# Kernel tuning notes

Hardware: AMD Instinct MI355X
Metric: run time of the kernel (lower is better)

Reference implementation:

```python
import jax, jax.numpy as jnp
import numpy as np
from jax import lax

DN = ('NCHW', 'OIHW', 'NCHW')


def _conv(x, w, b, stride, pad):
    y = lax.conv_general_dilated(x, w, (stride, stride), [(pad, pad), (pad, pad)],
                                 dimension_numbers=DN)
    return y + b[None, :, None, None]


def _deconv(x, w, b, stride, pad):
    # torch ConvTranspose2d weight: (in, out, kH, kW). Equivalent forward conv:
    # flip spatially, swap in/out, dilate input by stride, pad by k-1-pad.
    k = w.shape[2]
    kern = jnp.flip(w, (2, 3)).transpose(1, 0, 2, 3)  # (out, in, kH, kW)
    p = k - 1 - pad
    y = lax.conv_general_dilated(x, kern, (1, 1), [(p, p), (p, p)],
                                 lhs_dilation=(stride, stride), dimension_numbers=DN)
    return y + b[None, :, None, None]


def setup_inputs() -> dict:
    key = jax.random.key(0)
    ks = jax.random.split(key, 16)
    s = 0.05
    D, K, H = 64, 512, 128  # embedding_dim, num_embeddings, hidden_channels
    inp = {
        'x': jax.random.uniform(ks[0], (16, 3, 256, 256), dtype=jnp.float32),
        'conv1_w': jax.random.normal(ks[1], (H, 3, 4, 4), jnp.float32) * s,
        'conv1_b': jnp.zeros((H,), jnp.float32),
        'conv2_w': jax.random.normal(ks[2], (H, H, 4, 4), jnp.float32) * s,
        'conv2_b': jnp.zeros((H,), jnp.float32),
        'conv3_w': jax.random.normal(ks[3], (D, H, 3, 3), jnp.float32) * s,
        'conv3_b': jnp.zeros((D,), jnp.float32),
        'emb': jax.random.normal(ks[4], (K, D), jnp.float32),
        'deconv1_w': jax.random.normal(ks[5], (D, H, 4, 4), jnp.float32) * s,
        'deconv1_b': jnp.zeros((H,), jnp.float32),
        'deconv2_w': jax.random.normal(ks[6], (H, H, 4, 4), jnp.float32) * s,
        'deconv2_b': jnp.zeros((H,), jnp.float32),
        'deconv3_w': jax.random.normal(ks[7], (H, 3, 3, 3), jnp.float32) * s,
        'deconv3_b': jnp.zeros((3,), jnp.float32),
    }
    return inp


def reference(x, conv1_w, conv1_b, conv2_w, conv2_b, conv3_w, conv3_b, emb,
              deconv1_w, deconv1_b, deconv2_w, deconv2_b, deconv3_w, deconv3_b):
    # Encoder
    h = jax.nn.relu(_conv(x, conv1_w, conv1_b, 2, 1))
    h = jax.nn.relu(_conv(h, conv2_w, conv2_b, 2, 1))
    z_e = _conv(h, conv3_w, conv3_b, 1, 1)  # (B, 64, 64, 64)

    # Vector quantizer (faithful to torch: flatten NCHW directly to (-1, D))
    D = emb.shape[1]
    flat = z_e.reshape(-1, D)  # (N, D)
    d = (jnp.sum(flat * flat, axis=1, keepdims=True)
         + jnp.sum(emb * emb, axis=1)
         - 2.0 * flat @ emb.T)  # (N, K)
    indices = jnp.argmin(d, axis=1)[:, None]  # (N, 1)
    z_q = emb[indices[:, 0]].reshape(z_e.shape)

    # Decoder
    g = jax.nn.relu(_deconv(z_q, deconv1_w, deconv1_b, 2, 1))
    g = jax.nn.relu(_deconv(g, deconv2_w, deconv2_b, 2, 1))
    x_recon = jax.nn.sigmoid(_deconv(g, deconv3_w, deconv3_b, 1, 1))
    return (x_recon, indices, z_q)
```

## Files before the change

### kernel.cpp

```cpp
#include <hip/hip_runtime.h>
#include <hip/hip_bf16.h>

#define DEV __device__ __forceinline__

typedef __attribute__((ext_vector_type(8))) short bf16x8;
typedef __attribute__((ext_vector_type(4))) float f32x4;
typedef __attribute__((ext_vector_type(4))) unsigned short u16x4;

#define MFMA16(a,b,c) __builtin_amdgcn_mfma_f32_16x16x32_bf16(a,b,c,0,0,0)

DEV unsigned short bfbits(float v){ __hip_bfloat16 h = __float2bfloat16(v); return *(unsigned short*)&h; }
DEV float bf2f(unsigned short u){ __hip_bfloat16 h = *(__hip_bfloat16*)&u; return __bfloat162float(h); }
DEV void split3(float v, unsigned short& h, unsigned short& m, unsigned short& l) {
  h = bfbits(v);        float r  = v - bf2f(h);
  m = bfbits(r);        float r2 = r - bf2f(m);
  l = bfbits(r2);
}
DEV uint4 zero4(){ uint4 z; z.x=0; z.y=0; z.z=0; z.w=0; return z; }
DEV void gload_lds16(const void* g, void* l) {
  __builtin_amdgcn_global_load_lds(
      (const __attribute__((address_space(1))) void*)g,
      (__attribute__((address_space(3))) void*)l, 16, 0, 0);
}

DEV void prep_deconv_img(int i, int CI, const float* __restrict__ w, unsigned short* __restrict__ w2) {
  const int nch = CI/16;
  int cil = i & 7, s = (i >> 3) & 7, co = (i >> 6) & 127, f = (i >> 13) & 1;
  int rest = i >> 14;
  int ch = rest % nch, e = rest / nch;
  int k = ch*64 + s*8 + cil;
  int ci = (k & 15) | ((k >> 6) << 4);
  int tap = (k >> 4) & 3, a = tap >> 1, b = tap & 1;
  float v = w[ (((long)ci*128 + co)*4 + (2*a+1-e))*4 + (2*b+1-f) ];
  w2[(long)(e*nch + ch)*16384 + ((long)(f*128 + co))*64 + ((s ^ (co&7))*8) + cil] = bfbits(v);
}
__global__ __launch_bounds__(256) void wprep_all(
    const float* __restrict__ c1w, float* __restrict__ w2c1,
    const float* __restrict__ c2w, unsigned short* __restrict__ w2c2,
    const float* __restrict__ c3w, unsigned short* __restrict__ w2c3,
    const float* __restrict__ d1w, unsigned short* __restrict__ w2d1,
    const float* __restrict__ d2w, unsigned short* __restrict__ w2d2,
    const float* __restrict__ d3w, unsigned short* __restrict__ w2d3,
    const float* __restrict__ emb, float* __restrict__ esq) {
  const int bx = blockIdx.x, t = threadIdx.x;
  if (bx < 24) {
    int i = bx*256 + t;
    if (i < 6144) {
      int tap = i & 15, ci = (i>>4) % 3, co = i / 48;
      w2c1[((long)ci*16 + tap)*128 + co] = c1w[i];
    }
  } else if (bx < 1048) {
    int i = (bx-24)*256 + t;
    int cil = i & 7, s = (i>>3) & 15, co = (i>>7) & 63;
    int ch = (i>>13) & 15, cog = i >> 17;
    int co_g = cog*64 + co, ci = ch*8 + cil, ky = s >> 2, kx = s & 3;
    float v = c2w[(((long)co_g*128 + ci)*4 + ky)*4 + kx];
    unsigned short h,m,l; split3(v,h,m,l);
    long base = (long)(cog*16 + ch)*24576 + ((long)co*16 + (s ^ (co&15)))*8 + cil;
    w2c2[base] = h; w2c2[base + 8192] = m; w2c2[base + 16384] = l;
  } else if (bx < 1432) {
    int i = (bx-1048)*256 + t;
    int k = i % 1536, co = i / 1536;
    int ch = k / 96, rem = k % 96;
    int tap = rem >> 3, cil = rem & 7;
    int ci = ch*8 + cil, ky = tap >> 2, kx = tap & 3;
    float v = (kx < 3) ? c3w[(((long)co*128 + ci)*3 + ky)*3 + kx] : 0.f;
    unsigned short h,m,l; split3(v,h,m,l);
    long base = (long)ch*24576 + ((long)co*16 + (tap ^ (co&15)))*8 + cil;
    w2c3[base] = h; w2c3[base + 8192] = m; w2c3[base + 16384] = l;
  } else if (bx < 1944) {
    prep_deconv_img((bx-1432)*256 + t, 64, d1w, w2d1);
  } else if (bx < 2968) {
    prep_deconv_img((bx-1944)*256 + t, 128, d2w, w2d2);
  } else if (bx < 3064) {
    int i = (bx-2968)*256 + t;
    if (i < 24576) {
      int k = i % 1536, co = i / 1536;
      int ch = k / 96, rem = k % 96;
      int tap = rem >> 3, cil = rem & 7;
      int ci = ch*8 + cil, ky = tap >> 2, kx = tap & 3;
      float v = (co < 3 && kx < 3) ? d3w[(((long)ci*3 + co)*3 + ky)*3 + kx] : 0.f;
      w2d3[i] = bfbits(v);
    }
  } else {
    int code = (bx-3064)*256 + t;
    if (code < 512) {
      const float4* ev = (const float4*)(emb + (long)code*64);
      float s = 0.f;
      #pragma unroll
      for (int q=0;q<16;q++){ float4 e4 = ev[q];
        s += e4.x*e4.x + e4.y*e4.y + e4.z*e4.z + e4.w*e4.w; }
      esq[code] = s;
    }
  }
}

__global__ __launch_bounds__(256) void conv1_split(
    const float* __restrict__ x, const float* __restrict__ w2,
    const float* __restrict__ bias, unsigned short* __restrict__ h1, long PS1) {
  __shared__ __align__(16) float sIn[3][18][20];
  __shared__ __align__(16) float sW[3*16*64];
  const int tid = threadIdx.x;
  const int b = blockIdx.z >> 1, cog = blockIdx.z & 1;
  const int co0 = cog*64;
  const int oy0 = blockIdx.y*8, ox0 = blockIdx.x*8;
  const int cg2 = tid >> 5;
  const int pg2 = tid & 31;
  const int r = pg2 >> 2, pxp = (pg2 & 3)*2;
  float acc[8][2];
  #pragma unroll
  for (int c=0;c<8;c++){ float bv = bias[co0 + cg2*8 + c];
    acc[c][0]=bv; acc[c][1]=bv; }
  const float* xb = x + (long)b*3*256*256;
  const int iy0 = 2*oy0 - 1, ix0 = 2*ox0 - 1;
  for (int t=tid; t<3*18*18; t+=256) {
    int xx = t%18, yy=(t/18)%18, ci=t/324;
    int gy = iy0+yy, gx = ix0+xx;
    float v = 0.f;
    if (gy>=0 && gy<256 && gx>=0 && gx<256) v = xb[((long)ci*256+gy)*256+gx];
    sIn[ci][yy][xx] = v;
  }
  for (int t=tid; t<3*16*64; t+=256) {
    sW[t] = w2[(long)(t>>6)*128 + co0 + (t&63)];
  }
  __syncthreads();
  for (int ci=0; ci<3; ci++) {
    #pragma unroll
    for (int ky=0;ky<4;ky++)
    #pragma unroll
    for (int kx=0;kx<4;kx++) {
      const float* wp = &sW[(ci*16 + ky*4+kx)*64 + cg2*8];
      float4 w0 = *(const float4*)wp;
      float4 w1 = *(const float4*)(wp+4);
      const int yy = 2*r + ky;
      #pragma unroll
      for (int p=0;p<2;p++) {
        float iv = sIn[ci][yy][2*(pxp+p)+kx];
        acc[0][p] += w0.x*iv; acc[1][p] += w0.y*iv;
        acc[2][p] += w0.z*iv; acc[3][p] += w0.w*iv;
        acc[4][p] += w1.x*iv; acc[5][p] += w1.y*iv;
        acc[6][p] += w1.z*iv; acc[7][p] += w1.w*iv;
      }
    }
  }
  const int chg = cog*8 + cg2;
  #pragma unroll
  for (int p=0;p<2;p++) {
    unsigned short th[8], tm[8], tl[8];
    #pragma unroll
    for (int c=0;c<8;c++) {
      float v = fmaxf(acc[c][p], 0.f);
      split3(v, th[c], tm[c], tl[c]);
    }
    long base = (((long)(b*128 + oy0+r)*16 + chg)*128 + ox0+pxp+p)*8;
    *(uint4*)(h1 + base)          = *(uint4*)th;
    *(uint4*)(h1 + PS1 + base)    = *(uint4*)tm;
    *(uint4*)(h1 + 2*PS1 + base)  = *(uint4*)tl;
  }
}

__global__ __launch_bounds__(256, 2) void conv2_mfma(
    const unsigned short* __restrict__ h1, long PS1,
    const unsigned short* __restrict__ w2,
    const float* __restrict__ bias,
    unsigned short* __restrict__ h2I) {
  __shared__ __align__(16) unsigned short sA[3][4][130][8];
  __shared__ __align__(16) unsigned short sB[24576];
  const int tid = threadIdx.x;
  const int oy = blockIdx.x, cog = blockIdx.y, b = blockIdx.z;
  const int wave = tid >> 6, lane = tid & 63;
  const int wr = wave >> 1, wc = wave & 1;
  const int col_l = lane & 15, kg = lane >> 4;
  const int iy0 = 2*oy - 1;
  f32x4 acc[2][2] = {};
  unsigned short* sAf = &sA[0][0][0][0];
  const unsigned short* bsrc = w2 + (long)cog*16*24576;

  int aOff[6], aLdsO[6]; bool aOk[6];
  #pragma unroll
  for (int j = 0; j < 6; ++j) {
    int idx = tid + j*256;
    int px = idx & 127, rr = (idx >> 7) & 3, pl = idx >> 9;
    int iy = iy0 + rr;
    aOk[j] = (iy >= 0 && iy < 128);
    aOff[j] = (int)(pl*PS1 + (long)(b*128 + (aOk[j]?iy:0))*16384 + px*8);
    aLdsO[j] = ((pl*4 + rr)*130 + px + 1)*8;
  }
  uint4 pA[6];
  #pragma unroll
  for (int j=0;j<6;j++)  pA[j] = aOk[j] ? *(const uint4*)(h1 + aOff[j]) : zero4();

  if (tid < 24) {
    int pl = tid>>3, rr=(tid>>1)&3, c=tid&1;
    *(uint4*)&sA[pl][rr][c?129:0][0] = zero4();
  }

  for (int ch = 0; ch < 16; ++ch) {
    __syncthreads();
    #pragma unroll
    for (int j=0;j<6;j++)  *(uint4*)(sAf + aLdsO[j]) = pA[j];
    #pragma unroll
    for (int j = 0; j < 12; ++j) {
      int blk = wave*12 + j;
      gload_lds16(bsrc + (long)ch*24576 + blk*512 + lane*8, &sB[blk*512]);
    }
    __syncthreads();
    if (ch < 15) {
      #pragma unroll
      for (int j=0;j<6;j++)  pA[j] = aOk[j] ? *(const uint4*)(h1 + aOff[j] + (ch+1)*1024) : zero4();
      __builtin_amdgcn_sched_barrier(0);
    }
    #pragma unroll
    for (int s = 0; s < 4; ++s) {
      bf16x8 aF[2][3]; bf16x8 bF[2][3];
      const int tap = s*4 + kg;
      #pragma unroll
      for (int mf = 0; mf < 2; ++mf) {
        int ox = wr*32 + mf*16 + col_l;
        #pragma unroll
        for (int pl = 0; pl < 3; ++pl)
          aF[mf][pl] = *(const bf16x8*)&sA[pl][s][2*ox + kg][0];
      }
      #pragma unroll
      for (int nf = 0; nf < 2; ++nf) {
        int co = wc*32 + nf*16 + col_l;
        int ba = (co*16 + (tap ^ (co&15)))*8;
        bF[nf][0] = *(const bf16x8*)&sB[ba];
        bF[nf][1] = *(const bf16x8*)&sB[ba + 8192];
        bF[nf][2] = *(const bf16x8*)&sB[ba + 16384];
      }
      __builtin_amdgcn_s_setprio(1);
      #pragma unroll
      for (int mf = 0; mf < 2; ++mf)
      #pragma unroll
      for (int nf = 0; nf < 2; ++nf) {
        f32x4 a = acc[mf][nf];
        a = MFMA16(aF[mf][0], bF[nf][0], a);
        a = MFMA16(aF[mf][0], bF[nf][1], a);
        a = MFMA16(aF[mf][1], bF[nf][0], a);
        a = MFMA16(aF[mf][0], bF[nf][2], a);
        a = MFMA16(aF[mf][2], bF[nf][0], a);
        a = MFMA16(aF[mf][1], bF[nf][1], a);
        acc[mf][nf] = a;
      }
      __builtin_amdgcn_s_setprio(0);
    }
  }
  __syncthreads();
  #pragma unroll
  for (int nf = 0; nf < 2; ++nf) {
    int co = wc*32 + nf*16 + col_l;
    float bv = bias[cog*64 + co];
    #pragma unroll
    for (int mf = 0; mf < 2; ++mf) {
      int px0 = wr*32 + mf*16 + kg*4;
      u16x4 oh, om, ol;
      #pragma unroll
      for (int r = 0; r < 4; ++r) {
        float v = fmaxf(acc[mf][nf][r] + bv, 0.f);
        unsigned short h,m,l; split3(v,h,m,l);
        oh[r]=h; om[r]=m; ol[r]=l;
      }
      *(u16x4*)&sB[(0*64 + co)*72 + px0] = oh;
      *(u16x4*)&sB[(1*64 + co)*72 + px0] = om;
      *(u16x4*)&sB[(2*64 + co)*72 + px0] = ol;
    }
  }
  __syncthreads();
  #pragma unroll
  for (int j = 0; j < 6; ++j) {
    int idx = tid + j*256;
    int pl = idx >> 9, ch = (idx >> 6) & 7, px = idx & 63;
    unsigned short tmp[8];
    #pragma unroll
    for (int c = 0; c < 8; ++c) tmp[c] = sB[(pl*64 + ch*8 + c)*72 + px];
    *(uint4*)(h2I + ((((long)(b*64 + oy)*3 + pl)*16 + cog*8 + ch)*64 + px)*8) = *(uint4*)tmp;
  }
}

__global__ __launch_bounds__(256, 2) void conv3_mfma(
    const unsigned short* __restrict__ h2I,
    const unsigned short* __restrict__ w2,
    const float* __restrict__ bias,
    unsigned short* __restrict__ zeH, unsigned short* __restrict__ zeM,
    unsigned short* __restrict__ zeL) {
  __shared__ __align__(16) unsigned short sA3[3][3][68][8];
  __shared__ __align__(16) unsigned short sB[24576];
  const int tid = threadIdx.x;
  const int oy = blockIdx.x, b = blockIdx.z;
  const int wave = tid >> 6, lane = tid & 63;
  const int wr = wave >> 1, wc = wave & 1;
  const int col_l = lane & 15, kg = lane >> 4;
  f32x4 acc[2][2] = {};
  if (tid < 27) {
    int row = tid/3, c = tid%3;
    int pl = row/3, rr = row%3;
    *(uint4*)&sA3[pl][rr][(c==0)?0:(64+c)][0] = zero4();
  }
  if (oy == 0 && tid < 192) {
    int pl = tid >> 6, px = tid & 63;
    *(uint4*)&sA3[pl][0][px+1][0] = zero4();
  }
  if (oy == 63 && tid < 192) {
    int pl = tid >> 6, px = tid & 63;
    *(uint4*)&sA3[pl][2][px+1][0] = zero4();
  }

  for (int ch = 0; ch < 16; ++ch) {
    __syncthreads();
    #pragma unroll
    for (int j = 0; j < 3; ++j) {
      int row = wave*3 + j;
      if (row < 9) {
        int pl = row/3, rr = row%3;
        int iy = oy + rr - 1;
        if (iy >= 0 && iy < 64)
          gload_lds16(h2I + ((((long)(b*64 + iy)*3 + pl)*16 + ch)*64)*8 + lane*8,
                      &sA3[pl][rr][1][0]);
      }
    }
    #pragma unroll
    for (int j = 0; j < 12; ++j) {
      int blk = wave*12 + j;
      gload_lds16(w2 + (long)ch*24576 + blk*512 + lane*8, &sB[blk*512]);
    }
    __syncthreads();
    #pragma unroll
    for (int s = 0; s < 3; ++s) {
      bf16x8 aF[2][3]; bf16x8 bF[2][3];
      const int tap = s*4 + kg;
      #pragma unroll
      for (int mf = 0; mf < 2; ++mf) {
        int ox = wr*32 + mf*16 + col_l;
        #pragma unroll
        for (int pl = 0; pl < 3; ++pl)
          aF[mf][pl] = *(const bf16x8*)&sA3[pl][s][ox + kg][0];
      }
      #pragma unroll
      for (int nf = 0; nf < 2; ++nf) {
        int co = wc*32 + nf*16 + col_l;
        int ba = (co*16 + (tap ^ (co&15)))*8;
        bF[nf][0] = *(const bf16x8*)&sB[ba];
        bF[nf][1] = *(const bf16x8*)&sB[ba + 8192];
        bF[nf][2] = *(const bf16x8*)&sB[ba + 16384];
      }
      __builtin_amdgcn_s_setprio(1);
      #pragma unroll
      for (int mf = 0; mf < 2; ++mf)
      #pragma unroll
      for (int nf = 0; nf < 2; ++nf) {
        f32x4 a = acc[mf][nf];
        a = MFMA16(aF[mf][0], bF[nf][0], a);
        a = MFMA16(aF[mf][0], bF[nf][1], a);
        a = MFMA16(aF[mf][1], bF[nf][0], a);
        a = MFMA16(aF[mf][0], bF[nf][2], a);
        a = MFMA16(aF[mf][2], bF[nf][0], a);
        a = MFMA16(aF[mf][1], bF[nf][1], a);
        acc[mf][nf] = a;
      }
      __builtin_amdgcn_s_setprio(0);
    }
  }
  __syncthreads();
  #pragma unroll
  for (int nf = 0; nf < 2; ++nf) {
    int co = wc*32 + nf*16 + col_l;
    float bv = bias[co];
    #pragma unroll
    for (int mf = 0; mf < 2; ++mf) {
      int px0 = wr*32 + mf*16 + kg*4;
      u16x4 oh, om, ol;
      #pragma unroll
      for (int r = 0; r < 4; ++r) {
        float v = acc[mf][nf][r] + bv;
        unsigned short h,m,l; split3(v,h,m,l);
        oh[r]=h; om[r]=m; ol[r]=l;
      }
      *(u16x4*)&sB[(0*64 + co)*72 + px0] = oh;
      *(u16x4*)&sB[(1*64 + co)*72 + px0] = om;
      *(u16x4*)&sB[(2*64 + co)*72 + px0] = ol;
    }
  }
  __syncthreads();
  #pragma unroll
  for (int j = 0; j < 6; ++j) {
    int idx = tid + j*256;
    int pl = idx >> 9, co_l = (idx >> 3) & 63, q = idx & 7;
    uint4 v = *(const uint4*)&sB[(pl*64 + co_l)*72 + q*8];
    unsigned short* dst = (pl==0) ? zeH : ((pl==1) ? zeM : zeL);
    *(uint4*)(dst + ((long)(b*64 + co_l)*64 + oy)*64 + q*8) = v;
  }
}

template<int TX, int MODE>
struct SmemD {
  union {
    struct { __align__(16) unsigned short In[2][TX+2][24];
             __align__(16) unsigned short W[2*128*64]; } o;
    struct { __align__(16) unsigned short In[2][TX+2][16];
             __align__(16) unsigned short W[2*128*64]; } v;
    __align__(16) unsigned short Out[128][136];
  };
};

template<int CIN, int TX, int MODE>
__global__ __launch_bounds__(TX*4, (TX==64)?3:4) void deconv_mfma(
    const void* __restrict__ xin, const unsigned short* __restrict__ w2,
    const float* __restrict__ bias, unsigned short* __restrict__ yI) {
  constexpr int NTHR = TX*4;
  constexpr int NWAVE = NTHR/64;
  constexpr int NWG  = 32/NWAVE;
  __shared__ SmemD<TX,MODE> sm;
  unsigned short* Wb = MODE ? &sm.v.W[0] : &sm.o.W[0];

  const int tid = threadIdx.x;
  const int ty = blockIdx.x, e = blockIdx.y, b = blockIdx.z;
  const int wave = tid >> 6, lane = tid & 63;
  const int wc = wave & 1, wr = wave >> 1;
  const int f = (wr*64) / TX;
  const int tx_base = (wr*64) & (TX-1);
  const int col_l = lane & 15, kg = lane >> 4;
  const unsigned short* wsrc = w2 + (long)e*(CIN/16)*16384;

  constexpr int TPR = NTHR/32;
  const int rowid = tid / TPR, liO = tid % TPR;
  const int sci = rowid >> 1, srr = rowid & 1;
  float4 pLo, pHi; uint4 pIn;
  long aBase = 0; bool aOk = false;
  int pxV = 0, halfV = 0, rrV = 0;
  if (MODE == 0) {
    int iy = ty + e - 1 + srr;
    aOk = (iy >= 0 && iy < TX);
    aBase = ((long)b*CIN + sci)*TX*TX + (long)(aOk?iy:0)*TX + liO*8;
    if (aOk) { const float4* s4 = (const float4*)((const float*)xin + aBase);
               pLo = s4[0]; pHi = s4[1]; }
  } else {
    halfV = tid & 1; pxV = (tid >> 1) & (TX-1); rrV = tid >> 8;
    int iy = ty + e - 1 + rrV;
    aOk = (iy >= 0 && iy < TX);
    aBase = ((long)b*TX + (aOk?iy:0))*((long)(CIN/8)*TX*8) + (long)halfV*TX*8 + pxV*8;
    pIn = aOk ? *(const uint4*)((const unsigned short*)xin + aBase) : zero4();
  }

  if (MODE == 0) {
    if (tid < 64) {
      int rr = tid & 1, cc = ((tid>>1)&1) ? TX+1 : 0, ci = tid >> 2;
      sm.o.In[rr][cc][ci] = 0;
    }
  } else {
    if (tid < 8) {
      int rr = tid & 1, c = (tid>>1)&1, hf = (tid>>2)&1;
      *(uint4*)&sm.v.In[rr][c?TX+1:0][hf*8] = zero4();
    }
  }

  f32x4 acc[4][4] = {};
  for (int ch = 0; ch < CIN/16; ++ch) {
    __syncthreads();
    if (MODE == 0) {
      unsigned short vals[8];
      if (aOk) {
        float4 lo = pLo, hi = pHi;
        vals[0]=bfbits(lo.x); vals[1]=bfbits(lo.y); vals[2]=bfbits(lo.z); vals[3]=bfbits(lo.w);
        vals[4]=bfbits(hi.x); vals[5]=bfbits(hi.y); vals[6]=bfbits(hi.z); vals[7]=bfbits(hi.w);
      } else {
        #pragma unroll
        for (int j=0;j<8;j++) vals[j] = 0;
      }
      #pragma unroll
      for (int j=0;j<8;j++) {
        int jj = (j + liO) & 7;
        sm.o.In[srr][1 + liO*8 + jj][sci] = vals[jj];
      }
    } else {
      *(uint4*)&sm.v.In[rrV][pxV+1][halfV*8] = pIn;
    }
    #pragma unroll
    for (int j = 0; j < NWG; ++j) {
      int blk = wave*NWG + j;
      gload_lds16(wsrc + (long)ch*16384 + blk*512 + lane*8, Wb + blk*512);
    }
    __syncthreads();
    if (ch + 1 < CIN/16) {
      if (MODE == 0) {
        if (aOk) { const float4* s4 = (const float4*)((const float*)xin + aBase + (long)(ch+1)*16*TX*TX);
                   pLo = s4[0]; pHi = s4[1]; }
      } else {
        pIn = aOk ? *(const uint4*)((const unsigned short*)xin + aBase + (ch+1)*2*TX*8) : zero4();
      }
      __builtin_amdgcn_sched_barrier(0);
    }
    #pragma unroll
    for (int kk = 0; kk < 2; ++kk) {
      bf16x8 aF[4];
      const int tap = kk*2 + (kg >> 1), a = tap >> 1, bb = tap & 1;
      #pragma unroll
      for (int mf = 0; mf < 4; ++mf) {
        int tx = tx_base + mf*16 + col_l;
        if (MODE == 0) aF[mf] = *(const bf16x8*)&sm.o.In[1-a][tx + 1 + f - bb][(kg&1)*8];
        else           aF[mf] = *(const bf16x8*)&sm.v.In[1-a][tx + 1 + f - bb][(kg&1)*8];
      }
      const int slot = kk*4 + kg;
      __builtin_amdgcn_s_setprio(1);
      #pragma unroll
      for (int nf = 0; nf < 4; ++nf) {
        int co_l = nf*16 + col_l;
        bf16x8 bF = *(const bf16x8*)(Wb + (f*128 + wc*64 + co_l)*64 + (slot ^ (co_l & 7))*8);
        #pragma unroll
        for (int mf = 0; mf < 4; ++mf)
          acc[mf][nf] = MFMA16(aF[mf], bF, acc[mf][nf]);
      }
      __builtin_amdgcn_s_setprio(0);
    }
  }

  __syncthreads();
  float bv[4];
  #pragma unroll
  for (int nf = 0; nf < 4; ++nf) bv[nf] = bias[wc*64 + nf*16 + col_l];
  const int oy = 2*ty + e;
  if constexpr (TX == 64) {
    #pragma unroll
    for (int mf = 0; mf < 4; ++mf)
    #pragma unroll
    for (int nf = 0; nf < 4; ++nf) {
      int co = wc*64 + nf*16 + col_l;
      #pragma unroll
      for (int r = 0; r < 4; ++r) {
        int tx = tx_base + mf*16 + kg*4 + r;
        float v = fmaxf(acc[mf][nf][r] + bv[nf], 0.f);
        int ox = 2*tx + f;
        sm.Out[ox][co ^ (((ox>>3)&7)<<3)] = bfbits(v);
      }
    }
    __syncthreads();
    #pragma unroll
    for (int j = 0; j < 8; ++j) {
      int i = tid + j*NTHR;
      int px = i & 127, chn = i >> 7;
      uint4 vv = *(const uint4*)&sm.Out[px][(chn*8) ^ (((px>>3)&7)<<3)];
      *(uint4*)(yI + ((((long)b*128 + oy)*16 + chn)*128 + px)*8) = vv;
    }
  } else {
    const int myp = wr & 1;
    #pragma unroll
    for (int p = 0; p < 2; ++p) {
      if (myp == p) {
        #pragma unroll
        for (int mf = 0; mf < 4; ++mf)
        #pragma unroll
        for (int nf = 0; nf < 4; ++nf) {
          int co = wc*64 + nf*16 + col_l;
          #pragma unroll
          for (int r = 0; r < 4; ++r) {
            int tx = tx_base + mf*16 + kg*4 + r;
            float v = fmaxf(acc[mf][nf][r] + bv[nf], 0.f);
            int ox = 2*tx + f;
            sm.Out[ox & 127][co ^ (((ox>>3)&7)<<3)] = bfbits(v);
          }
        }
      }
      __syncthreads();
      #pragma unroll
      for (int j = 0; j < 4; ++j) {
        int i = tid + j*NTHR;
        int px = i & 127, chn = i >> 7;
        uint4 vv = *(const uint4*)&sm.Out[px][(chn*8) ^ (((px>>3)&7)<<3)];
        int pxg = p*128 + px;
        *(uint4*)(yI + ((((long)b*256 + oy)*16 + chn)*256 + pxg)*8) = vv;
      }
      if (p == 0) __syncthreads();
    }
  }
}

__global__ __launch_bounds__(256, 2) void deconv3_mfma(
    const unsigned short* __restrict__ g2I,
    const unsigned short* __restrict__ w2,
    const float* __restrict__ bias, float* __restrict__ y) {
  __shared__ __align__(16) unsigned short sA[3][260][8];
  __shared__ __align__(16) unsigned short sB[16*12*16*8];
  const int tid = threadIdx.x;
  const int oy = blockIdx.x, b = blockIdx.y;
  const int wave = tid >> 6, lane = tid & 63;
  const int col_l = lane & 15, kg = lane >> 4;
  const int pxb = wave*64;
  for (int i = tid; i < 3072; i += 256) {
    int co = i & 15, tap = (i>>4) % 12, ch = i/192;
    *(uint4*)&sB[((ch*12+tap)*16+co)*8] = *(const uint4*)(w2 + (long)co*1536 + ch*96 + tap*8);
  }
  if (tid < 12) {
    int dy = tid >> 2, c = tid & 3;
    *(uint4*)&sA[dy][(c<2)?c:(256+c)][0] = zero4();
  }
  long aBase[3]; int aLdsO[3]; bool aOk[3];
  #pragma unroll
  for (int u = 0; u < 3; ++u) {
    int idx = tid + u*256;
    int px = idx & 255, dy = idx >> 8;
    int iy = oy - 1 + dy;
    aOk[u] = (iy >= 0 && iy < 256);
    aBase[u] = ((long)(b*256 + (aOk[u]?iy:0)))*32768 + px*8;
    aLdsO[u] = (dy*260 + px + 2)*8;
  }
  uint4 pA[3];
  #pragma unroll
  for (int u=0;u<3;u++) pA[u] = aOk[u] ? *(const uint4*)(g2I + aBase[u]) : zero4();

  unsigned short* sAf = &sA[0][0][0];
  f32x4 acc[4] = {};
  for (int ch = 0; ch < 16; ++ch) {
    __syncthreads();
    #pragma unroll
    for (int u=0;u<3;u++) *(uint4*)(sAf + aLdsO[u]) = pA[u];
    __syncthreads();
    if (ch < 15) {
      #pragma unroll
      for (int u=0;u<3;u++)
        pA[u] = aOk[u] ? *(const uint4*)(g2I + aBase[u] + (ch+1)*2048) : zero4();
      __builtin_amdgcn_sched_barrier(0);
    }
    #pragma unroll
    for (int s = 0; s < 3; ++s) {
      bf16x8 bF = *(const bf16x8*)&sB[((ch*12 + s*4 + kg)*16 + col_l)*8];
      __builtin_amdgcn_s_setprio(1);
      #pragma unroll
      for (int mf = 0; mf < 4; ++mf) {
        int px = pxb + mf*16 + col_l;
        bf16x8 aF = *(const bf16x8*)&sA[2-s][px + 3 - kg][0];
        acc[mf] = MFMA16(aF, bF, acc[mf]);
      }
      __builtin_amdgcn_s_setprio(0);
    }
  }
  if (col_l < 3) {
    float bv = bias[col_l];
    #pragma unroll
    for (int mf = 0; mf < 4; ++mf) {
      int px = pxb + mf*16 + kg*4;
      float4 o;
      o.x = 1.f/(1.f + expf(-(acc[mf][0] + bv)));
      o.y = 1.f/(1.f + expf(-(acc[mf][1] + bv)));
      o.z = 1.f/(1.f + expf(-(acc[mf][2] + bv)));
      o.w = 1.f/(1.f + expf(-(acc[mf][3] + bv)));
      *(float4*)(y + ((long)(b*3 + col_l)*256 + oy)*256 + px) = o;
    }
  }
}

__global__ __launch_bounds__(256, 2) void vq_mfma(
    const unsigned short* __restrict__ zeH, const unsigned short* __restrict__ zeM,
    const unsigned short* __restrict__ zeL,
    const float* __restrict__ emb, const float* __restrict__ esq,
    float* __restrict__ out_idx, float* __restrict__ zq) {
  __shared__ __align__(16) unsigned short sA[64*3*8*8];
  __shared__ __align__(16) unsigned short sB[128*3*8*8];
  __shared__ float snb[128];
  __shared__ int sidx[64];
  const int tid = threadIdx.x;
  const long n0 = (long)blockIdx.x*64;
  const int wave = tid >> 6, lane = tid & 63;
  const int col = lane & 15, kg = lane >> 4;

  #pragma unroll
  for (int j = 0; j < 6; ++j) {
    int idx = tid + j*256;
    int pl = idx >> 9, rem = idx & 511;
    int n = rem >> 3, slot = rem & 7;
    const unsigned short* src = (pl==0 ? zeH : (pl==1 ? zeM : zeL)) + (n0+n)*64 + slot*8;
    *(uint4*)&sA[((n*3 + pl)*8 + (slot ^ (n&7)))*8] = *(const uint4*)src;
  }

  const int codeT = tid >> 1, halfT = tid & 1;
  float4 pB[8];
  #pragma unroll
  for (int q = 0; q < 8; ++q)
    pB[q] = *(const float4*)(emb + (long)codeT*64 + halfT*32 + q*4);
  float pSn = (tid < 128) ? esq[tid] : 0.f;

  float best[4] = {3.4e38f,3.4e38f,3.4e38f,3.4e38f};
  int bidx[4] = {0,0,0,0};

  for (int ch = 0; ch < 4; ++ch) {
    __syncthreads();
    #pragma unroll
    for (int s4 = 0; s4 < 4; ++s4) {
      int slot = halfT*4 + s4;
      float4 lo = pB[s4*2], hi = pB[s4*2+1];
      unsigned short th[8], tm[8], tl[8];
      split3(lo.x, th[0], tm[0], tl[0]); split3(lo.y, th[1], tm[1], tl[1]);
      split3(lo.z, th[2], tm[2], tl[2]); split3(lo.w, th[3], tm[3], tl[3]);
      split3(hi.x, th[4], tm[4], tl[4]); split3(hi.y, th[5], tm[5], tl[5]);
      split3(hi.z, th[6], tm[6], tl[6]); split3(hi.w, th[7], tm[7], tl[7]);
      int base = ((codeT*3)*8 + (slot ^ (codeT&7)))*8;
      *(uint4*)&sB[base]       = *(uint4*)th;
      *(uint4*)&sB[base + 64]  = *(uint4*)tm;
      *(uint4*)&sB[base + 128] = *(uint4*)tl;
    }
    if (tid < 128) snb[tid] = pSn;
    if (ch < 3) {
      #pragma unroll
      for (int q = 0; q < 8; ++q)
        pB[q] = *(const float4*)(emb + ((long)(ch+1)*128 + codeT)*64 + halfT*32 + q*4);
      if (tid < 128) pSn = esq[(ch+1)*128 + tid];
    }
    __syncthreads();

    f32x4 acc[8] = {};
    #pragma unroll
    for (int kk = 0; kk < 2; ++kk) {
      const int nloc = wave*16 + col;
      const int slot = kk*4 + kg;
      bf16x8 aF[3];
      #pragma unroll
      for (int pl = 0; pl < 3; ++pl)
        aF[pl] = *(const bf16x8*)&sA[((nloc*3 + pl)*8 + (slot ^ (nloc&7)))*8];
      __builtin_amdgcn_s_setprio(1);
      #pragma unroll
      for (int cf = 0; cf < 8; ++cf) {
        int cl = cf*16 + col;
        int bb = ((cl*3)*8 + (slot ^ (cl&7)))*8;
        bf16x8 b0 = *(const bf16x8*)&sB[bb];
        bf16x8 b1 = *(const bf16x8*)&sB[bb + 64];
        bf16x8 b2 = *(const bf16x8*)&sB[bb + 128];
        f32x4 a = acc[cf];
        a = MFMA16(aF[0], b0, a);
        a = MFMA16(aF[0], b1, a);
        a = MFMA16(aF[1], b0, a);
        a = MFMA16(aF[0], b2, a);
        a = MFMA16(aF[2], b0, a);
        a = MFMA16(aF[1], b1, a);
        acc[cf] = a;
      }
      __builtin_amdgcn_s_setprio(0);
    }
    #pragma unroll
    for (int cf = 0; cf < 8; ++cf) {
      float sv = snb[cf*16 + col];
      int code = ch*128 + cf*16 + col;
      #pragma unroll
      for (int j = 0; j < 4; ++j) {
        float s = sv - 2.f*acc[cf][j];
        if (s < best[j]) { best[j] = s; bidx[j] = code; }
      }
    }
  }

  #pragma unroll
  for (int j = 0; j < 4; ++j) {
    float b = best[j]; int ii = bidx[j];
    #pragma unroll
    for (int off = 1; off < 16; off <<= 1) {
      float ob = __shfl_xor(b, off);
      int oi = __shfl_xor(ii, off);
      if (ob < b || (ob == b && oi < ii)) { b = ob; ii = oi; }
    }
    if (col == 0) sidx[wave*16 + kg*4 + j] = ii;
  }
  __syncthreads();
  if (tid < 64) out_idx[n0 + tid] = (float)sidx[tid];
  #pragma unroll
  for (int j = 0; j < 4; ++j) {
    int t = tid + j*256;
    int row = t >> 4, q = t & 15;
    float4 v = *(const float4*)(emb + (long)sidx[row]*64 + q*4);
    *(float4*)(zq + (n0 + row)*64 + q*4) = v;
  }
}

extern "C" void kernel_launch(void* const* d_in, const int* in_sizes, int n_in,
                              void* d_out, int out_size, void* d_ws, size_t ws_size,
                              hipStream_t stream) {
  const float* x   = (const float*)d_in[0];
  const float* c1w = (const float*)d_in[1];  const float* c1b = (const float*)d_in[2];
  const float* c2w = (const float*)d_in[3];  const float* c2b = (const float*)d_in[4];
  const float* c3w = (const float*)d_in[5];  const float* c3b = (const float*)d_in[6];
  const float* emb = (const float*)d_in[7];
  const float* d1w = (const float*)d_in[8];  const float* d1b = (const float*)d_in[9];
  const float* d2w = (const float*)d_in[10]; const float* d2b = (const float*)d_in[11];
  const float* d3w = (const float*)d_in[12]; const float* d3b = (const float*)d_in[13];
  float* out = (float*)d_out;

  float* xrec = out;
  float* oidx = out + 3145728;
  float* zq   = out + 3211264;

  const long XB  = 196608;
  const long ZEB = 262144;
  const long PS1 = 8388608;
  const long H2B = 1572864;

  const size_t NEEDED = 112273408ULL;
  if (ws_size < NEEDED) return;
  char* wsb = (char*)d_ws;
  unsigned short* h1grp = (unsigned short*)wsb;
  unsigned short* g2grp = (unsigned short*)wsb;
  unsigned short* h2I   = (unsigned short*)(wsb + 67108864);
  unsigned short* g1grp = (unsigned short*)(wsb + 67108864);
  unsigned short* zeH = (unsigned short*)(wsb + 92274688);
  unsigned short* zeM = (unsigned short*)(wsb + 100663296);
  unsigned short* zeL = (unsigned short*)out;
  char* W = wsb + 109051904;
  float* w2c1          = (float*)(W);
  unsigned short* w2c2 = (unsigned short*)(W + 24576);
  unsigned short* w2c3 = (unsigned short*)(W + 1597440);
  unsigned short* w2d1 = (unsigned short*)(W + 2383872);
  unsigned short* w2d2 = (unsigned short*)(W + 2646016);
  unsigned short* w2d3 = (unsigned short*)(W + 3170304);
  float* esq           = (float*)(W + 3219456);

  wprep_all<<<3066, 256, 0, stream>>>(c1w, w2c1, c2w, w2c2, c3w, w2c3,
                                      d1w, w2d1, d2w, w2d2, d3w, w2d3, emb, esq);

  for (int g = 0; g < 4; ++g) {
    conv1_split<<<dim3(16,16,8), 256, 0, stream>>>(
        x + (long)g*4*XB, w2c1, c1b, h1grp, PS1);
    conv2_mfma<<<dim3(64,2,4), 256, 0, stream>>>(
        h1grp, PS1, w2c2, c2b, h2I + (long)(g&1)*4*H2B);
    if (g & 1) {
      long zo = (long)(g>>1)*8*ZEB;
      conv3_mfma<<<dim3(64,1,8), 256, 0, stream>>>(
          h2I, w2c3, c3b, zeH + zo, zeM + zo, zeL + zo);
    }
  }
  vq_mfma<<<1024, 256, 0, stream>>>(zeH, zeM, zeL, emb, esq, oidx, zq);

  for (int g = 0; g < 4; ++g) {
    deconv_mfma<64, 64, 0 ><<<dim3(64, 2, 4), 256, 0, stream>>>(
        (const void*)(zq + (long)g*4*ZEB), w2d1, d1b, g1grp);
    deconv_mfma<128,128,1 ><<<dim3(128,2,4), 512, 0, stream>>>(
        (const void*)g1grp, w2d2, d2b, g2grp);
    deconv3_mfma<<<dim3(256,4), 256, 0, stream>>>(
        g2grp, w2d3, d3b, xrec + (long)g*4*XB);
  }
}
```

Before: 744.5 us.

## Compute two output rows per deconv3 block and batch decoder in groups of eight

Measured after the change: 672.4 us. -9.7%, faster.

```diff
diff --git a/kernel.cpp b/kernel.cpp
--- a/kernel.cpp
+++ b/kernel.cpp
@@ -574,49 +574,50 @@
   }
 }
 
-__global__ __launch_bounds__(256, 2) void deconv3_mfma(
+__global__ __launch_bounds__(512, 4) void deconv3_mfma(
     const unsigned short* __restrict__ g2I,
     const unsigned short* __restrict__ w2,
     const float* __restrict__ bias, float* __restrict__ y) {
-  __shared__ __align__(16) unsigned short sA[3][260][8];
+  __shared__ __align__(16) unsigned short sA[4][260][8];
   __shared__ __align__(16) unsigned short sB[16*12*16*8];
   const int tid = threadIdx.x;
-  const int oy = blockIdx.x, b = blockIdx.y;
+  const int oy0 = blockIdx.x*2, b = blockIdx.y;
   const int wave = tid >> 6, lane = tid & 63;
   const int col_l = lane & 15, kg = lane >> 4;
-  const int pxb = wave*64;
-  for (int i = tid; i < 3072; i += 256) {
+  const int r = wave >> 2;
+  const int pxb = (wave & 3)*64;
+  for (int i = tid; i < 3072; i += 512) {
     int co = i & 15, tap = (i>>4) % 12, ch = i/192;
     *(uint4*)&sB[((ch*12+tap)*16+co)*8] = *(const uint4*)(w2 + (long)co*1536 + ch*96 + tap*8);
   }
-  if (tid < 12) {
+  if (tid < 16) {
     int dy = tid >> 2, c = tid & 3;
     *(uint4*)&sA[dy][(c<2)?c:(256+c)][0] = zero4();
   }
-  long aBase[3]; int aLdsO[3]; bool aOk[3];
-  #pragma unroll
-  for (int u = 0; u < 3; ++u) {
-    int idx = tid + u*256;
+  long aBase[2]; int aLdsO[2]; bool aOk[2];
+  #pragma unroll
+  for (int u = 0; u < 2; ++u) {
+    int idx = tid + u*512;
     int px = idx & 255, dy = idx >> 8;
-    int iy = oy - 1 + dy;
+    int iy = oy0 - 1 + dy;
     aOk[u] = (iy >= 0 && iy < 256);
     aBase[u] = ((long)(b*256 + (aOk[u]?iy:0)))*32768 + px*8;
     aLdsO[u] = (dy*260 + px + 2)*8;
   }
-  uint4 pA[3];
-  #pragma unroll
-  for (int u=0;u<3;u++) pA[u] = aOk[u] ? *(const uint4*)(g2I + aBase[u]) : zero4();
+  uint4 pA[2];
+  #pragma unroll
+  for (int u=0;u<2;u++) pA[u] = aOk[u] ? *(const uint4*)(g2I + aBase[u]) : zero4();
 
   unsigned short* sAf = &sA[0][0][0];
   f32x4 acc[4] = {};
   for (int ch = 0; ch < 16; ++ch) {
     __syncthreads();
     #pragma unroll
-    for (int u=0;u<3;u++) *(uint4*)(sAf + aLdsO[u]) = pA[u];
+    for (int u=0;u<2;u++) *(uint4*)(sAf + aLdsO[u]) = pA[u];
     __syncthreads();
     if (ch < 15) {
       #pragma unroll
-      for (int u=0;u<3;u++)
+      for (int u=0;u<2;u++)
         pA[u] = aOk[u] ? *(const uint4*)(g2I + aBase[u] + (ch+1)*2048) : zero4();
       __builtin_amdgcn_sched_barrier(0);
     }
@@ -627,13 +628,14 @@
       #pragma unroll
       for (int mf = 0; mf < 4; ++mf) {
         int px = pxb + mf*16 + col_l;
-        bf16x8 aF = *(const bf16x8*)&sA[2-s][px + 3 - kg][0];
+        bf16x8 aF = *(const bf16x8*)&sA[r + 2 - s][px + 3 - kg][0];
         acc[mf] = MFMA16(aF, bF, acc[mf]);
       }
       __builtin_amdgcn_s_setprio(0);
     }
   }
   if (col_l < 3) {
+    const int oy = oy0 + r;
     float bv = bias[col_l];
     #pragma unroll
     for (int mf = 0; mf < 4; ++mf) {
@@ -790,17 +792,17 @@
   const long PS1 = 8388608;
   const long H2B = 1572864;
 
-  const size_t NEEDED = 112273408ULL;
+  const size_t NEEDED  = 112273408ULL;
+  const size_t NEEDED8 = 170994688ULL;
   if (ws_size < NEEDED) return;
+  const bool use8 = (ws_size >= NEEDED8);
   char* wsb = (char*)d_ws;
   unsigned short* h1grp = (unsigned short*)wsb;
-  unsigned short* g2grp = (unsigned short*)wsb;
   unsigned short* h2I   = (unsigned short*)(wsb + 67108864);
-  unsigned short* g1grp = (unsigned short*)(wsb + 67108864);
   unsigned short* zeH = (unsigned short*)(wsb + 92274688);
   unsigned short* zeM = (unsigned short*)(wsb + 100663296);
   unsigned short* zeL = (unsigned short*)out;
-  char* W = wsb + 109051904;
+  char* W = use8 ? (wsb + 167772160) : (wsb + 109051904);
   float* w2c1          = (float*)(W);
   unsigned short* w2c2 = (unsigned short*)(W + 24576);
   unsigned short* w2c3 = (unsigned short*)(W + 1597440);
@@ -825,12 +827,27 @@
   }
   vq_mfma<<<1024, 256, 0, stream>>>(zeH, zeM, zeL, emb, esq, oidx, zq);
 
-  for (int g = 0; g < 4; ++g) {
-    deconv_mfma<64, 64, 0 ><<<dim3(64, 2, 4), 256, 0, stream>>>(
-        (const void*)(zq + (long)g*4*ZEB), w2d1, d1b, g1grp);
-    deconv_mfma<128,128,1 ><<<dim3(128,2,4), 512, 0, stream>>>(
-        (const void*)g1grp, w2d2, d2b, g2grp);
-    deconv3_mfma<<<dim3(256,4), 256, 0, stream>>>(
-        g2grp, w2d3, d3b, xrec + (long)g*4*XB);
-  }
-}
+  if (use8) {
+    unsigned short* g2g = (unsigned short*)wsb;
+    unsigned short* g1g = (unsigned short*)(wsb + 134217728);
+    for (int g = 0; g < 2; ++g) {
+      deconv_mfma<64, 64, 0 ><<<dim3(64, 2, 8), 256, 0, stream>>>(
+          (const void*)(zq + (long)g*8*ZEB), w2d1, d1b, g1g);
+      deconv_mfma<128,128,1 ><<<dim3(128,2,8), 512, 0, stream>>>(
+          (const void*)g1g, w2d2, d2b, g2g);
+      deconv3_mfma<<<dim3(128,8), 512, 0, stream>>>(
+          g2g, w2d3, d3b, xrec + (long)g*8*XB);
+    }
+  } else {
+    unsigned short* g2g = (unsigned short*)wsb;
+    unsigned short* g1g = (unsigned short*)(wsb + 67108864);
+    for (int g = 0; g < 4; ++g) {
+      deconv_mfma<64, 64, 0 ><<<dim3(64, 2, 4), 256, 0, stream>>>(
+          (const void*)(zq + (long)g*4*ZEB), w2d1, d1b, g1g);
+      deconv_mfma<128,128,1 ><<<dim3(128,2,4), 512, 0, stream>>>(
+          (const void*)g1g, w2d2, d2b, g2g);
+      deconv3_mfma<<<dim3(128,4), 512, 0, stream>>>(
+          g2g, w2d3, d3b, xrec + (long)g*4*XB);
+    }
+  }
+}
```
